# Performance work log

Measured on AMD Instinct MI355X. Metric: run time of the kernel, lower is better.

Reference implementation:

```python
import jax, jax.numpy as jnp
import numpy as np

N, E, D_IN, D_HID, D_OUT, G = 50000, 800000, 64, 64, 64, 64
BN_EPS = 1e-5


def gcn_conv(x, W, b, src, dst, n_nodes):
    """PyG GCNConv: add self-loops, sym-normalized sum aggregation, then bias.
    out_i = sum_{j->i} d_j^-1/2 d_i^-1/2 (x W)_j + d_i^-1 (x W)_i + b
    where d_i = 1 + in-degree(i) (self-loop included)."""
    h = x @ W  # [N, out]
    deg = jax.ops.segment_sum(jnp.ones((src.shape[0],), h.dtype), dst,
                              num_segments=n_nodes) + 1.0  # self-loop
    dinv = jax.lax.rsqrt(deg)  # deg >= 1 always
    coef = dinv[src] * dinv[dst]  # [E]
    msgs = h[src] * coef[:, None]  # [E, out] -- the big gather
    agg = jax.ops.segment_sum(msgs, dst, num_segments=n_nodes)
    agg = agg + h * (dinv * dinv)[:, None]  # self-loop messages
    return agg + b


def global_mean_pool(x, batch, n_graphs):
    sums = jax.ops.segment_sum(x, batch, num_segments=n_graphs)
    cnts = jax.ops.segment_sum(jnp.ones((x.shape[0],), x.dtype), batch,
                               num_segments=n_graphs)
    return sums / jnp.maximum(cnts, 1.0)[:, None]


def setup_inputs() -> dict:
    key = jax.random.key(0)
    ks = jax.random.split(key, 8)
    x = jax.random.normal(ks[0], (N, D_IN), dtype=jnp.float32)
    edge_index = jax.random.randint(ks[1], (2, E), 0, N, dtype=jnp.int32)
    batch = jnp.sort(jax.random.randint(ks[2], (N,), 0, G, dtype=jnp.int32))
    s1 = 1.0 / np.sqrt(D_IN)
    s2 = 1.0 / np.sqrt(D_HID)
    W1 = jax.random.uniform(ks[3], (D_IN, D_HID), jnp.float32, -s1, s1)
    b1 = jnp.zeros((D_HID,), jnp.float32)
    gamma = jnp.ones((D_HID,), jnp.float32)
    beta = jnp.zeros((D_HID,), jnp.float32)
    W2 = jax.random.uniform(ks[4], (D_HID, D_OUT), jnp.float32, -s2, s2)
    b2 = jnp.zeros((D_OUT,), jnp.float32)
    return {"x": x, "edge_index": edge_index, "batch": batch,
            "W1": W1, "b1": b1, "gamma": gamma, "beta": beta,
            "W2": W2, "b2": b2}


def reference(x, edge_index, batch, W1, b1, gamma, beta, W2, b2):
    src, dst = edge_index[0], edge_index[1]
    h = gcn_conv(x, W1, b1, src, dst, N)
    # BatchNorm1d with batch statistics (training-mode forward)
    mu = jnp.mean(h, axis=0)
    var = jnp.mean(jnp.square(h - mu), axis=0)
    h = (h - mu) * jax.lax.rsqrt(var + BN_EPS) * gamma + beta
    h = jax.nn.elu(h)
    # dropout is identity in eval / deterministic reference
    out = gcn_conv(h, W2, b2, src, dst, N)
    graph_rep = global_mean_pool(out, batch, G)
    return (out, graph_rep)
```

## Files before the change

### kernel.cpp

```cpp
#include <hip/hip_runtime.h>


constexpr int GGRAPHS = 64;
constexpr int EPB = 8192;

__global__ void cnt_kernel(const int* __restrict__ batch, int* __restrict__ cnt, int n) {
  __shared__ int h[GGRAPHS];
  int t = threadIdx.x;
  if (t < GGRAPHS) h[t] = 0;
  __syncthreads();
  for (int i = blockIdx.x * 256 + t; i < n; i += gridDim.x * 256) {
    int g = batch[i];
    if ((unsigned)g < (unsigned)GGRAPHS) atomicAdd(&h[g], 1);
  }
  __syncthreads();
  if (t < GGRAPHS && h[t] > 0) atomicAdd(&cnt[t], h[t]);
}

__global__ void phist_kernel(const int* __restrict__ dst, int* __restrict__ hist,
                             int E, int n, int nblk, int nbuck) {
  __shared__ int h[256];
  int t = threadIdx.x;
  h[t] = 0;
  __syncthreads();
  int e0 = blockIdx.x * EPB;
  int e1 = e0 + EPB < E ? e0 + EPB : E;
  for (int i = e0 + t; i < e1; i += 256) {
    int d = dst[i];
    if ((unsigned)d < (unsigned)n) atomicAdd(&h[d >> 8], 1);
  }
  __syncthreads();
  if (t < nbuck) hist[t * nblk + blockIdx.x] = h[t];
}

__global__ void scan1_kernel(const int* __restrict__ in, int* __restrict__ out,
                             int* __restrict__ bsum, int n) {
  __shared__ int tmp[256];
  int t = threadIdx.x;
  int i = blockIdx.x * 256 + t;
  int v = (i < n) ? in[i] : 0;
  tmp[t] = v;
  __syncthreads();
#pragma unroll
  for (int off = 1; off < 256; off <<= 1) {
    int a = (t >= off) ? tmp[t - off] : 0;
    __syncthreads();
    tmp[t] += a;
    __syncthreads();
  }
  if (i < n) out[i] = tmp[t] - v;
  if (t == 255) bsum[blockIdx.x] = tmp[255];
}

__global__ void scan2_kernel(int* __restrict__ bsum, int nb) {
  __shared__ int tmp[256];
  int t = threadIdx.x;
  int v = (t < nb) ? bsum[t] : 0;
  tmp[t] = v;
  __syncthreads();
#pragma unroll
  for (int off = 1; off < 256; off <<= 1) {
    int a = (t >= off) ? tmp[t - off] : 0;
    __syncthreads();
    tmp[t] += a;
    __syncthreads();
  }
  if (t < nb) bsum[t] = tmp[t] - v;
  if (t == 255) bsum[nb] = tmp[255];
}

__global__ void scan_add_kernel(int* __restrict__ data, const int* __restrict__ bsum,
                                int S, int nbt) {
  int i = blockIdx.x * 256 + threadIdx.x;
  if (i < S) data[i] += bsum[blockIdx.x];
  if (i == 0) data[S] = bsum[nbt];
}

__global__ void part_kernel(const int* __restrict__ srcp, const int* __restrict__ dstp,
                            const int* __restrict__ hist, int* __restrict__ part,
                            int E, int n, int nblk, int nbuck) {
  __shared__ int cur[256];
  int t = threadIdx.x;
  if (t < nbuck) cur[t] = hist[t * nblk + blockIdx.x];
  __syncthreads();
  int e0 = blockIdx.x * EPB;
  int e1 = e0 + EPB < E ? e0 + EPB : E;
  for (int i = e0 + t; i < e1; i += 256) {
    int d = dstp[i];
    if ((unsigned)d >= (unsigned)n) continue;
    int s = srcp[i];
    int pos = atomicAdd(&cur[d >> 8], 1);
    part[pos] = (s << 8) | (d & 255);
  }
}

__global__ void csr_kernel(const int* __restrict__ part, const int* __restrict__ hist,
                           int* __restrict__ rowptr, float* __restrict__ dinv,
                           int* __restrict__ col, int n, int nblk, int nbuck) {
  __shared__ int degL[256], scn[256], cur[256];
  int t = threadIdx.x;
  int b = blockIdx.x;
  degL[t] = 0;
  cur[t] = 0;
  __syncthreads();
  int base = hist[b * nblk];
  int end = hist[(b + 1) * nblk];
  for (int i = base + t; i < end; i += 256) atomicAdd(&degL[part[i] & 255], 1);
  __syncthreads();
  int dv = degL[t];
  scn[t] = dv;
  __syncthreads();
#pragma unroll
  for (int off = 1; off < 256; off <<= 1) {
    int a = (t >= off) ? scn[t - off] : 0;
    __syncthreads();
    scn[t] += a;
    __syncthreads();
  }
  int excl = scn[t] - dv;
  int node = (b << 8) + t;
  if (node < n) {
    rowptr[node] = base + excl;
    dinv[node] = rsqrtf((float)dv + 1.0f);
  }
  if (b == nbuck - 1 && t == 0) rowptr[n] = end;
  scn[t] = excl;
  __syncthreads();
  for (int i = base + t; i < end; i += 256) {
    int u = part[i];
    int d = u & 255;
    int k = atomicAdd(&cur[d], 1);
    col[base + scn[d] + k] = u >> 8;
  }
}

__global__ void mm64_kernel(const float* __restrict__ X, const float* __restrict__ W,
                            float* __restrict__ Y, int n) {
  __shared__ float Ws[64][64];
  __shared__ float xs[4][64];
  int tid = threadIdx.x;
  for (int i = tid; i < 64 * 64; i += 256) Ws[i >> 6][i & 63] = W[i];
  int rr = tid >> 6, c = tid & 63;
  int row = blockIdx.x * 4 + rr;
  xs[rr][c] = (row < n) ? X[(size_t)row * 64 + c] : 0.0f;
  __syncthreads();
  float acc = 0.0f;
#pragma unroll
  for (int k = 0; k < 64; ++k) acc = fmaf(xs[rr][k], Ws[k][c], acc);
  if (row < n) Y[(size_t)row * 64 + c] = acc;
}

__global__ void bn_elu_mm64_kernel(const float* __restrict__ X, const float* __restrict__ W,
                                   const float* __restrict__ ss, float* __restrict__ Y, int n) {
  __shared__ float Ws[64][64];
  __shared__ float xs[4][64];
  int tid = threadIdx.x;
  for (int i = tid; i < 64 * 64; i += 256) Ws[i >> 6][i & 63] = W[i];
  int rr = tid >> 6, c = tid & 63;
  int row = blockIdx.x * 4 + rr;
  float v = 0.0f;
  if (row < n) {
    v = X[(size_t)row * 64 + c] * ss[c] + ss[64 + c];
    v = v > 0.0f ? v : expm1f(v);
  }
  xs[rr][c] = v;
  __syncthreads();
  float acc = 0.0f;
#pragma unroll
  for (int k = 0; k < 64; ++k) acc = fmaf(xs[rr][k], Ws[k][c], acc);
  if (row < n) Y[(size_t)row * 64 + c] = acc;
}

__device__ __forceinline__ float4 gcn_gather_core(
    const int* __restrict__ rowptr, const int* __restrict__ col,
    const float* __restrict__ dinv, const float4* __restrict__ H4,
    int row, int lane, int sub, int cg, bool valid) {
  float4 acc = make_float4(0.f, 0.f, 0.f, 0.f);
  int p0 = 0, p1 = 0;
  if (valid) { p0 = rowptr[row]; p1 = rowptr[row + 1]; }
  for (int base = p0; base < p1; base += 64) {
    int myp = base + lane;
    int j = (myp < p1) ? col[myp] : 0;
    float w = (myp < p1) ? dinv[j] : 0.0f;
    int m = p1 - base;
    m = m < 64 ? m : 64;
#pragma unroll 4
    for (int k = 0; k < m; k += 4) {
      int s = k + sub;
      int jj = __shfl(j, s);
      float ww = __shfl(w, s);
      float4 hv = H4[(size_t)jj * 16 + cg];
      acc.x = fmaf(hv.x, ww, acc.x);
      acc.y = fmaf(hv.y, ww, acc.y);
      acc.z = fmaf(hv.z, ww, acc.z);
      acc.w = fmaf(hv.w, ww, acc.w);
    }
  }
  acc.x += __shfl_xor(acc.x, 16);
  acc.y += __shfl_xor(acc.y, 16);
  acc.z += __shfl_xor(acc.z, 16);
  acc.w += __shfl_xor(acc.w, 16);
  acc.x += __shfl_xor(acc.x, 32);
  acc.y += __shfl_xor(acc.y, 32);
  acc.z += __shfl_xor(acc.z, 32);
  acc.w += __shfl_xor(acc.w, 32);
  return acc;
}

__global__ void gather_bn_kernel(const int* __restrict__ rowptr, const int* __restrict__ col,
                                 const float* __restrict__ dinv, const float* __restrict__ H,
                                 const float* __restrict__ b, float* __restrict__ OUT,
                                 float* __restrict__ bnsR, int n) {
  int wave = threadIdx.x >> 6;
  int lane = threadIdx.x & 63;
  int row = blockIdx.x * 4 + wave;
  bool valid = row < n;
  int sub = lane >> 4;
  int cg = lane & 15;
  const float4* __restrict__ H4 = (const float4*)H;
  float4 acc = gcn_gather_core(rowptr, col, dinv, H4, row, lane, sub, cg, valid);
  float4 o = make_float4(0.f, 0.f, 0.f, 0.f);
  if (valid) {
    float di = dinv[row];
    float d2 = di * di;
    float4 self = H4[(size_t)row * 16 + cg];
    float4 bb = ((const float4*)b)[cg];
    o.x = fmaf(acc.x, di, fmaf(self.x, d2, bb.x));
    o.y = fmaf(acc.y, di, fmaf(self.y, d2, bb.y));
    o.z = fmaf(acc.z, di, fmaf(self.z, d2, bb.z));
    o.w = fmaf(acc.w, di, fmaf(self.w, d2, bb.w));
    if (sub == 0) ((float4*)OUT)[(size_t)row * 16 + cg] = o;
  }
  __shared__ float sA[4][64], sB[4][64];
  if (sub == 0) {
    sA[wave][4 * cg + 0] = o.x;
    sA[wave][4 * cg + 1] = o.y;
    sA[wave][4 * cg + 2] = o.z;
    sA[wave][4 * cg + 3] = o.w;
    sB[wave][4 * cg + 0] = o.x * o.x;
    sB[wave][4 * cg + 1] = o.y * o.y;
    sB[wave][4 * cg + 2] = o.z * o.z;
    sB[wave][4 * cg + 3] = o.w * o.w;
  }
  __syncthreads();
  int t = threadIdx.x;
  if (t < 64) {
    float s = sA[0][t] + sA[1][t] + sA[2][t] + sA[3][t];
    float s2 = sB[0][t] + sB[1][t] + sB[2][t] + sB[3][t];
    float* d = bnsR + (size_t)(blockIdx.x & 255) * 128;
    atomicAdd(&d[t], s);
    atomicAdd(&d[64 + t], s2);
  }
}

__global__ void gather_pool_kernel(const int* __restrict__ rowptr, const int* __restrict__ col,
                                   const float* __restrict__ dinv, const float* __restrict__ H,
                                   const float* __restrict__ b, float* __restrict__ OUT,
                                   const int* __restrict__ batch, float* __restrict__ poolR,
                                   int n) {
  int wave = threadIdx.x >> 6;
  int lane = threadIdx.x & 63;
  int row = blockIdx.x * 4 + wave;
  bool valid = row < n;
  int sub = lane >> 4;
  int cg = lane & 15;
  const float4* __restrict__ H4 = (const float4*)H;
  float4 acc = gcn_gather_core(rowptr, col, dinv, H4, row, lane, sub, cg, valid);
  float4 o = make_float4(0.f, 0.f, 0.f, 0.f);
  __shared__ float sO[4][64];
  __shared__ int sG[4];
  if (valid) {
    float di = dinv[row];
    float d2 = di * di;
    float4 self = H4[(size_t)row * 16 + cg];
    float4 bb = ((const float4*)b)[cg];
    o.x = fmaf(acc.x, di, fmaf(self.x, d2, bb.x));
    o.y = fmaf(acc.y, di, fmaf(self.y, d2, bb.y));
    o.z = fmaf(acc.z, di, fmaf(self.z, d2, bb.z));
    o.w = fmaf(acc.w, di, fmaf(self.w, d2, bb.w));
    if (sub == 0) ((float4*)OUT)[(size_t)row * 16 + cg] = o;
  }
  if (lane == 0) {
    int g = valid ? batch[row] : -1;
    sG[wave] = ((unsigned)g < (unsigned)GGRAPHS) ? g : -1;
  }
  if (sub == 0) {
    sO[wave][4 * cg + 0] = o.x;
    sO[wave][4 * cg + 1] = o.y;
    sO[wave][4 * cg + 2] = o.z;
    sO[wave][4 * cg + 3] = o.w;
  }
  __syncthreads();
  int t = threadIdx.x;
  if (t < 64) {
    float* base = poolR + (size_t)(blockIdx.x & 15) * 4096;
    int g0 = sG[0];
    float s0 = 0.0f;
#pragma unroll
    for (int w = 0; w < 4; ++w) {
      int gw = sG[w];
      if (gw < 0) continue;
      if (gw == g0) s0 += sO[w][t];
      else atomicAdd(&base[gw * 64 + t], sO[w][t]);
    }
    if (g0 >= 0) atomicAdd(&base[g0 * 64 + t], s0);
  }
}

__global__ void bn_final_kernel(const float* __restrict__ bnsR, const float* __restrict__ gamma,
                                const float* __restrict__ beta, float* __restrict__ ss, int n) {
  __shared__ float red[128];
  int t = threadIdx.x;
  float s = 0.0f;
  for (int r = 0; r < 256; ++r) s += bnsR[r * 128 + t];
  red[t] = s;
  __syncthreads();
  if (t < 64) {
    float inv_n = 1.0f / (float)n;
    float mu = red[t] * inv_n;
    float var = red[64 + t] * inv_n - mu * mu;
    var = fmaxf(var, 0.0f);
    float sc = gamma[t] * rsqrtf(var + 1e-5f);
    ss[t] = sc;
    ss[64 + t] = beta[t] - mu * sc;
  }
}

__global__ void pool_final_kernel(const float* __restrict__ poolR, const int* __restrict__ cnt,
                                  float* __restrict__ out) {
  int idx = blockIdx.x * 256 + threadIdx.x;
  float s = 0.0f;
  for (int r = 0; r < 16; ++r) s += poolR[r * 4096 + idx];
  int g = idx >> 6;
  float c = (float)cnt[g];
  out[idx] = s / fmaxf(c, 1.0f);
}

extern "C" void kernel_launch(void* const* d_in, const int* in_sizes, int n_in,
                              void* d_out, int out_size, void* d_ws, size_t ws_size,
                              hipStream_t stream) {
  const float* x = (const float*)d_in[0];
  const int* ei = (const int*)d_in[1];
  const int* batch = (const int*)d_in[2];
  const float* W1 = (const float*)d_in[3];
  const float* b1 = (const float*)d_in[4];
  const float* gamma = (const float*)d_in[5];
  const float* beta = (const float*)d_in[6];
  const float* W2 = (const float*)d_in[7];
  const float* b2 = (const float*)d_in[8];

  const int n = in_sizes[0] / 64;
  const int E = in_sizes[1] / 2;
  const int* srcp = ei;
  const int* dstp = ei + E;

  float* ws = (float*)d_ws;
  size_t nf = (size_t)n * 64;
  float* bufA = ws;
  float* bufB = ws + nf;
  float* dinv = ws + 2 * nf;
  float* ss = dinv + n;
  int* rowptr = (int*)(ss + 128);
  int* col = rowptr + n + 1;
  int* bsum = col + E;
  float* bnsR = (float*)(bsum + 257);
  float* poolR = bnsR + 256 * 128;
  int* cnti = (int*)(poolR + 16 * 4096);

  int* part = (int*)bufA;
  int* hist = part + E;

  float* out = (float*)d_out;

  size_t zbytes = (size_t)((char*)(cnti + 64) - (char*)bnsR);
  hipMemsetAsync(bnsR, 0, zbytes, stream);

  int blk = 256;
  int nblkP = (E + EPB - 1) / EPB;
  int nbuck = (n + 255) >> 8;
  int S = nbuck * nblkP;
  int nbt = (S + 255) / 256;
  int gridRows = (n + 3) / 4;

  phist_kernel<<<nblkP, blk, 0, stream>>>(dstp, hist, E, n, nblkP, nbuck);
  cnt_kernel<<<128, blk, 0, stream>>>(batch, cnti, n);
  scan1_kernel<<<nbt, blk, 0, stream>>>(hist, hist, bsum, S);
  scan2_kernel<<<1, blk, 0, stream>>>(bsum, nbt);
  scan_add_kernel<<<nbt, blk, 0, stream>>>(hist, bsum, S, nbt);
  part_kernel<<<nblkP, blk, 0, stream>>>(srcp, dstp, hist, part, E, n, nblkP, nbuck);
  csr_kernel<<<nbuck, blk, 0, stream>>>(part, hist, rowptr, dinv, col, n, nblkP, nbuck);

  mm64_kernel<<<gridRows, blk, 0, stream>>>(x, W1, bufA, n);
  gather_bn_kernel<<<gridRows, blk, 0, stream>>>(rowptr, col, dinv, bufA, b1, bufB, bnsR, n);
  bn_final_kernel<<<1, 128, 0, stream>>>(bnsR, gamma, beta, ss, n);
  bn_elu_mm64_kernel<<<gridRows, blk, 0, stream>>>(bufB, W2, ss, bufA, n);
  gather_pool_kernel<<<gridRows, blk, 0, stream>>>(rowptr, col, dinv, bufA, b2, out, batch,
                                                   poolR, n);
  pool_final_kernel<<<16, blk, 0, stream>>>(poolR, cnti, out + nf);
}
```

Measured before the change: 276.2 us.

## Merge histogram, graph count and first matmul into one launch

Combines the dst-bucket histogram, the per-graph node count and the first 64x64 matmul into a single kernel whose blocks pick a role from their block index. To make that possible, the part/hist scratch arrays move out of bufA (which the matmul now writes at the same time) into their own workspace region. The goal is to cut two kernel launches and let the independent passes overlap on the GPU. In exchange, every block reserves the largest shared-memory footprint of the three roles, and the workspace grows.

```diff
diff --git a/kernel.cpp b/kernel.cpp
--- a/kernel.cpp
+++ b/kernel.cpp
@@ -3,34 +3,53 @@
 
 constexpr int GGRAPHS = 64;
 constexpr int EPB = 8192;
-
-__global__ void cnt_kernel(const int* __restrict__ batch, int* __restrict__ cnt, int n) {
-  __shared__ int h[GGRAPHS];
-  int t = threadIdx.x;
-  if (t < GGRAPHS) h[t] = 0;
-  __syncthreads();
-  for (int i = blockIdx.x * 256 + t; i < n; i += gridDim.x * 256) {
-    int g = batch[i];
-    if ((unsigned)g < (unsigned)GGRAPHS) atomicAdd(&h[g], 1);
-  }
-  __syncthreads();
-  if (t < GGRAPHS && h[t] > 0) atomicAdd(&cnt[t], h[t]);
-}
-
-__global__ void phist_kernel(const int* __restrict__ dst, int* __restrict__ hist,
-                             int E, int n, int nblk, int nbuck) {
+constexpr int CNTB = 128;
+
+__global__ void fat_phist_cnt_mm64_kernel(
+    const int* __restrict__ dst, const int* __restrict__ batch,
+    int* __restrict__ hist, int* __restrict__ cnt,
+    const float* __restrict__ X, const float* __restrict__ W,
+    float* __restrict__ Y,
+    int E, int n, int nblk, int nbuck) {
+  __shared__ float Ws[64][64];
+  __shared__ float xs[4][64];
   __shared__ int h[256];
-  int t = threadIdx.x;
-  h[t] = 0;
-  __syncthreads();
-  int e0 = blockIdx.x * EPB;
-  int e1 = e0 + EPB < E ? e0 + EPB : E;
-  for (int i = e0 + t; i < e1; i += 256) {
-    int d = dst[i];
-    if ((unsigned)d < (unsigned)n) atomicAdd(&h[d >> 8], 1);
-  }
-  __syncthreads();
-  if (t < nbuck) hist[t * nblk + blockIdx.x] = h[t];
+  __shared__ int hb[GGRAPHS];
+  int t = threadIdx.x;
+  int bid = blockIdx.x;
+  if (bid < nblk) {
+    h[t] = 0;
+    __syncthreads();
+    int e0 = bid * EPB;
+    int e1 = e0 + EPB < E ? e0 + EPB : E;
+    for (int i = e0 + t; i < e1; i += 256) {
+      int d = dst[i];
+      if ((unsigned)d < (unsigned)n) atomicAdd(&h[d >> 8], 1);
+    }
+    __syncthreads();
+    if (t < nbuck) hist[t * nblk + bid] = h[t];
+  } else if (bid < nblk + CNTB) {
+    int cb = bid - nblk;
+    if (t < GGRAPHS) hb[t] = 0;
+    __syncthreads();
+    for (int i = cb * 256 + t; i < n; i += CNTB * 256) {
+      int g = batch[i];
+      if ((unsigned)g < (unsigned)GGRAPHS) atomicAdd(&hb[g], 1);
+    }
+    __syncthreads();
+    if (t < GGRAPHS && hb[t] > 0) atomicAdd(&cnt[t], hb[t]);
+  } else {
+    int mb = bid - nblk - CNTB;
+    for (int i = t; i < 64 * 64; i += 256) Ws[i >> 6][i & 63] = W[i];
+    int rr = t >> 6, c = t & 63;
+    int row = mb * 4 + rr;
+    xs[rr][c] = (row < n) ? X[(size_t)row * 64 + c] : 0.0f;
+    __syncthreads();
+    float acc = 0.0f;
+#pragma unroll
+    for (int k = 0; k < 64; ++k) acc = fmaf(xs[rr][k], Ws[k][c], acc);
+    if (row < n) Y[(size_t)row * 64 + c] = acc;
+  }
 }
 
 __global__ void scan1_kernel(const int* __restrict__ in, int* __restrict__ out,
@@ -132,22 +151,6 @@
     int k = atomicAdd(&cur[d], 1);
     col[base + scn[d] + k] = u >> 8;
   }
-}
-
-__global__ void mm64_kernel(const float* __restrict__ X, const float* __restrict__ W,
-                            float* __restrict__ Y, int n) {
-  __shared__ float Ws[64][64];
-  __shared__ float xs[4][64];
-  int tid = threadIdx.x;
-  for (int i = tid; i < 64 * 64; i += 256) Ws[i >> 6][i & 63] = W[i];
-  int rr = tid >> 6, c = tid & 63;
-  int row = blockIdx.x * 4 + rr;
-  xs[rr][c] = (row < n) ? X[(size_t)row * 64 + c] : 0.0f;
-  __syncthreads();
-  float acc = 0.0f;
-#pragma unroll
-  for (int k = 0; k < 64; ++k) acc = fmaf(xs[rr][k], Ws[k][c], acc);
-  if (row < n) Y[(size_t)row * 64 + c] = acc;
 }
 
 __global__ void bn_elu_mm64_kernel(const float* __restrict__ X, const float* __restrict__ W,
@@ -354,6 +357,12 @@
   const int* srcp = ei;
   const int* dstp = ei + E;
 
+  int nblkP = (E + EPB - 1) / EPB;
+  int nbuck = (n + 255) >> 8;
+  int S = nbuck * nblkP;
+  int nbt = (S + 255) / 256;
+  int gridRows = (n + 3) / 4;
+
   float* ws = (float*)d_ws;
   size_t nf = (size_t)n * 64;
   float* bufA = ws;
@@ -362,35 +371,29 @@
   float* ss = dinv + n;
   int* rowptr = (int*)(ss + 128);
   int* col = rowptr + n + 1;
-  int* bsum = col + E;
+  int* part = col + E;
+  int* hist = part + E;
+  int* bsum = hist + S + 1;
   float* bnsR = (float*)(bsum + 257);
   float* poolR = bnsR + 256 * 128;
   int* cnti = (int*)(poolR + 16 * 4096);
 
-  int* part = (int*)bufA;
-  int* hist = part + E;
-
   float* out = (float*)d_out;
 
   size_t zbytes = (size_t)((char*)(cnti + 64) - (char*)bnsR);
   hipMemsetAsync(bnsR, 0, zbytes, stream);
 
   int blk = 256;
-  int nblkP = (E + EPB - 1) / EPB;
-  int nbuck = (n + 255) >> 8;
-  int S = nbuck * nblkP;
-  int nbt = (S + 255) / 256;
-  int gridRows = (n + 3) / 4;
-
-  phist_kernel<<<nblkP, blk, 0, stream>>>(dstp, hist, E, n, nblkP, nbuck);
-  cnt_kernel<<<128, blk, 0, stream>>>(batch, cnti, n);
+  int fatGrid = nblkP + CNTB + gridRows;
+
+  fat_phist_cnt_mm64_kernel<<<fatGrid, blk, 0, stream>>>(
+      dstp, batch, hist, cnti, x, W1, bufA, E, n, nblkP, nbuck);
   scan1_kernel<<<nbt, blk, 0, stream>>>(hist, hist, bsum, S);
   scan2_kernel<<<1, blk, 0, stream>>>(bsum, nbt);
   scan_add_kernel<<<nbt, blk, 0, stream>>>(hist, bsum, S, nbt);
   part_kernel<<<nblkP, blk, 0, stream>>>(srcp, dstp, hist, part, E, n, nblkP, nbuck);
   csr_kernel<<<nbuck, blk, 0, stream>>>(part, hist, rowptr, dinv, col, n, nblkP, nbuck);
 
-  mm64_kernel<<<gridRows, blk, 0, stream>>>(x, W1, bufA, n);
   gather_bn_kernel<<<gridRows, blk, 0, stream>>>(rowptr, col, dinv, bufA, b1, bufB, bnsR, n);
   bn_final_kernel<<<1, 128, 0, stream>>>(bnsR, gamma, beta, ss, n);
   bn_elu_mm64_kernel<<<gridRows, blk, 0, stream>>>(bufB, W2, ss, bufA, n);
```

After: 267.0 us. 1.03x faster.
